# Performance work log

Hardware: AMD Instinct MI355X
Metric: run time of the kernel (lower is better)

## Reference

```python
import jax, jax.numpy as jnp
import numpy as np

PATCH = 16
TOP_K = 5
EPS = 1e-12


def l2_normalize(x, axis):
    sq = jnp.sum(x * x, axis=axis, keepdims=True)
    return x * jax.lax.rsqrt(jnp.maximum(sq, EPS))


def patch_embed(imgs, conv_w, conv_b):
    # imgs: (P, 3, 32, 32) -> (P, n_patches=4, D=768)
    y = jax.lax.conv_general_dilated(
        imgs, conv_w, window_strides=(PATCH, PATCH), padding='VALID',
        dimension_numbers=('NCHW', 'OIHW', 'NCHW'))  # (P, D, 2, 2)
    y = y + conv_b[None, :, None, None]
    P, D = y.shape[0], y.shape[1]
    return y.reshape(P, D, -1).transpose(0, 2, 1)  # (P, 4, D)


def setup_inputs() -> dict:
    key = jax.random.key(0)
    k1, k2, k3, k4 = jax.random.split(key, 4)
    B, N, D = 256, 196, 768
    P = 32  # pool_size
    x_embed = jax.random.normal(k1, (B, N, D), dtype=jnp.float32)
    # uniform(-1, 1) init as in the torch module
    prompt = jax.random.uniform(k2, (P, 3, 32, 32), dtype=jnp.float32, minval=-1.0, maxval=1.0)
    prompt_key = jax.random.uniform(k3, (P, D), dtype=jnp.float32, minval=-1.0, maxval=1.0)
    conv_w = jax.random.normal(k4, (D, 3, PATCH, PATCH), dtype=jnp.float32) * 0.02
    conv_b = jnp.zeros((D,), dtype=jnp.float32)
    return {'x_embed': x_embed, 'prompt': prompt, 'prompt_key': prompt_key,
            'conv_w': conv_w, 'conv_b': conv_b}


def reference(x_embed, prompt, prompt_key, conv_w, conv_b):
    B = x_embed.shape[0]
    prompt_embed = patch_embed(prompt, conv_w, conv_b)      # (P, 4, D)

    x_embed_mean = jnp.mean(x_embed, axis=1)                # (B, D), embedding_key='mean'
    prompt_norm = l2_normalize(prompt_key, axis=1)          # (P, D)
    x_embed_norm = l2_normalize(x_embed_mean, axis=1)       # (B, D)
    similarity = x_embed_norm @ prompt_norm.T               # (B, P)

    _, idx = jax.lax.top_k(similarity, TOP_K)               # (B, top_k)

    batched_prompt_embed = prompt_embed[idx]                # (B, top_k, 4, D)
    Bq, K, L, D = batched_prompt_embed.shape
    batched_prompt_embed = batched_prompt_embed.reshape(Bq, K * L, D)

    batched_key_norm = prompt_norm[idx]                     # (B, top_k, D)
    reduce_sim = jnp.sum(batched_key_norm * x_embed_norm[:, None, :]) / B

    prompted_embedding = jnp.concatenate([batched_prompt_embed, x_embed], axis=1)
    return prompted_embedding, reduce_sim, similarity, idx
```

## Files before the change

### kernel.cpp

```cpp
#include <hip/hip_runtime.h>

typedef float __attribute__((ext_vector_type(4))) f32x4;

#define BB 256
#define NN 196
#define DD 768
#define PP 32
#define TOPK 5
#define NROW 216

#define OUT0_ELTS (BB * NROW * DD)
#define RS_OFF    OUT0_ELTS
#define SIM_OFF   (OUT0_ELTS + 1)
#define IDX_OFF   (OUT0_ELTS + 1 + BB * PP)

#define WS_PEMB   0

__global__ __launch_bounds__(256) void k_prep(const float* __restrict__ prompt,
                                              const float* __restrict__ cw,
                                              const float* __restrict__ cb,
                                              float* __restrict__ pemb) {
    const int t = threadIdx.x;
    const int bxx = blockIdx.x;
    const int chunk = bxx / 32, pg = bxx - chunk * 32;
    const int m0 = pg * 4;
    const int n = chunk * 256 + t;
    __shared__ float patch[4 * DD];
    for (int idx = t; idx < 4 * DD; idx += 256) {
        const int j = idx / DD, kk = idx - j * DD;
        const int c = kk >> 8, rem = kk & 255;
        const int kh = rem >> 4, kw = rem & 15;
        const int m = m0 + j;
        const int p = m >> 2, l = m & 3;
        patch[idx] = prompt[(size_t)p * 3072 + (size_t)c * 1024
                            + ((l >> 1) * 16 + kh) * 32 + (l & 1) * 16 + kw];
    }
    __syncthreads();
    const float4* wrow = (const float4*)(cw + (size_t)n * DD);
    const float4* p0 = (const float4*)(patch);
    const float4* p1 = (const float4*)(patch + DD);
    const float4* p2 = (const float4*)(patch + 2 * DD);
    const float4* p3 = (const float4*)(patch + 3 * DD);
    float a0 = 0.f, a1 = 0.f, a2 = 0.f, a3 = 0.f;
#pragma unroll 4
    for (int kk = 0; kk < 192; ++kk) {
        const float4 w = wrow[kk];
        const float4 q0 = p0[kk], q1 = p1[kk], q2 = p2[kk], q3 = p3[kk];
        a0 += q0.x * w.x + q0.y * w.y + q0.z * w.z + q0.w * w.w;
        a1 += q1.x * w.x + q1.y * w.y + q1.z * w.z + q1.w * w.w;
        a2 += q2.x * w.x + q2.y * w.y + q2.z * w.z + q2.w * w.w;
        a3 += q3.x * w.x + q3.y * w.y + q3.z * w.z + q3.w * w.w;
    }
    const float bias = cb[n];
    pemb[(size_t)(m0 + 0) * DD + n] = a0 + bias;
    pemb[(size_t)(m0 + 1) * DD + n] = a1 + bias;
    pemb[(size_t)(m0 + 2) * DD + n] = a2 + bias;
    pemb[(size_t)(m0 + 3) * DD + n] = a3 + bias;
}

__global__ __launch_bounds__(768) void k_fused(const float* __restrict__ x,
                                               const float* __restrict__ pkey,
                                               const float* __restrict__ pemb,
                                               float* __restrict__ out) {
    const int b = blockIdx.x;
    const int t = threadIdx.x;
    const int g = t / 192, c = t - g * 192;
    const float* xb = x + (size_t)b * (NN * DD);
    float* ob = out + (size_t)b * (NROW * DD) + 20 * DD;
    f32x4 s = (f32x4)(0.f);
    f32x4 va[7], vb[7];
#pragma unroll
    for (int i = 0; i < 7; ++i)
        va[i] = __builtin_nontemporal_load((const f32x4*)(xb + (size_t)(g + 4 * i) * DD) + c);
#pragma unroll
    for (int o = 0; o < 7; ++o) {
        if (o < 6) {
#pragma unroll
            for (int i = 0; i < 7; ++i) {
                const int row = g + 4 * ((o + 1) * 7 + i);
                vb[i] = __builtin_nontemporal_load((const f32x4*)(xb + (size_t)row * DD) + c);
            }
        }
#pragma unroll
        for (int i = 0; i < 7; ++i) {
            const int row = g + 4 * (o * 7 + i);
            s += va[i];
            __builtin_nontemporal_store(va[i], (f32x4*)(ob + (size_t)row * DD) + c);
        }
#pragma unroll
        for (int i = 0; i < 7; ++i) va[i] = vb[i];
    }
    __shared__ f32x4 comb[768];
    __shared__ float xm[768];
    __shared__ float sims[PP];
    __shared__ float wred[12];
    __shared__ float rsh;
    __shared__ int lidx[TOPK];
    comb[g * 192 + c] = s;
    __syncthreads();
    if (g == 0) {
        f32x4 s0 = comb[c], s1 = comb[192 + c], s2 = comb[384 + c], s3 = comb[576 + c];
        f32x4 m4 = (s0 + s1 + s2 + s3) * (1.0f / NN);
        xm[4 * c + 0] = m4.x;
        xm[4 * c + 1] = m4.y;
        xm[4 * c + 2] = m4.z;
        xm[4 * c + 3] = m4.w;
    }
    __syncthreads();
    float sq = xm[t] * xm[t];
#pragma unroll
    for (int off = 32; off; off >>= 1) sq += __shfl_down(sq, off);
    if ((t & 63) == 0) wred[t >> 6] = sq;
    __syncthreads();
    if (t == 0) {
        float tot = 0.f;
        for (int i = 0; i < 12; ++i) tot += wred[i];
        rsh = rsqrtf(fmaxf(tot, 1e-12f));
    }
    __syncthreads();
    const float r = rsh;
    if (t < 512) {
        const int p = t >> 4, sub = t & 15;
        const float* pr = pkey + (size_t)p * DD;
        float acc = 0.f, nrm = 0.f;
#pragma unroll 8
        for (int j = 0; j < 48; ++j) {
            const int k = sub + (j << 4);
            const float pk = pr[k];
            acc += xm[k] * pk;
            nrm += pk * pk;
        }
        acc += __shfl_down(acc, 8, 16);  nrm += __shfl_down(nrm, 8, 16);
        acc += __shfl_down(acc, 4, 16);  nrm += __shfl_down(nrm, 4, 16);
        acc += __shfl_down(acc, 2, 16);  nrm += __shfl_down(nrm, 2, 16);
        acc += __shfl_down(acc, 1, 16);  nrm += __shfl_down(nrm, 1, 16);
        if (sub == 0) {
            const float sv = acc * rsqrtf(fmaxf(nrm, 1e-12f)) * r;
            sims[p] = sv;
            out[SIM_OFF + b * PP + p] = sv;
        }
    }
    __syncthreads();
    if (t < 64) {
        float v = (t < PP) ? sims[t] : -1e30f;
        float rsum = 0.f;
#pragma unroll
        for (int k = 0; k < TOPK; ++k) {
            float bv = v; int bbi = t;
#pragma unroll
            for (int off = 32; off; off >>= 1) {
                const float ov = __shfl_xor(bv, off);
                const int   oi = __shfl_xor(bbi, off);
                if (ov > bv || (ov == bv && oi < bbi)) { bv = ov; bbi = oi; }
            }
            if (t == 0) {
                lidx[k] = bbi;
                out[IDX_OFF + b * TOPK + k] = (float)bbi;
                rsum += bv;
            }
            if (t == bbi) v = -1e30f;
        }
        if (t == 0) atomicAdd(&out[RS_OFF], rsum * (1.0f / BB));
    }
    __syncthreads();
    f32x4* dst = (f32x4*)(out + (size_t)b * (NROW * DD));
    const f32x4* src = (const f32x4*)pemb;
    for (int v = t; v < 20 * 192; v += 768) {
        const int row = v / 192;
        const int off = v - row * 192;
        const int srow = lidx[row >> 2] * 4 + (row & 3);
        __builtin_nontemporal_store(src[srow * 192 + off], dst + row * 192 + off);
    }
}

extern "C" void kernel_launch(void* const* d_in, const int* in_sizes, int n_in,
                              void* d_out, int out_size, void* d_ws, size_t ws_size,
                              hipStream_t stream) {
    const float* x      = (const float*)d_in[0];
    const float* prompt = (const float*)d_in[1];
    const float* pkey   = (const float*)d_in[2];
    const float* cw     = (const float*)d_in[3];
    const float* cb     = (const float*)d_in[4];
    float* out = (float*)d_out;
    char* ws = (char*)d_ws;

    float* pemb = (float*)(ws + WS_PEMB);

    hipMemsetAsync(out + RS_OFF, 0, sizeof(float), stream);
    k_prep<<<96, 256, 0, stream>>>(prompt, cw, cb, pemb);
    k_fused<<<BB, 768, 0, stream>>>(x, pkey, pemb, out);
}
```

Baseline: 331.3 us.

## Split row copy across two blocks per batch and merge patch-embed into copy kernel

```diff
diff --git a/kernel.cpp b/kernel.cpp
--- a/kernel.cpp
+++ b/kernel.cpp
@@ -16,98 +16,97 @@
 
 #define WS_PEMB   0
 
-__global__ __launch_bounds__(256) void k_prep(const float* __restrict__ prompt,
-                                              const float* __restrict__ cw,
-                                              const float* __restrict__ cb,
-                                              float* __restrict__ pemb) {
+__global__ __launch_bounds__(768, 6) void k_copy(
+    const float* __restrict__ x, const float* __restrict__ prompt,
+    const float* __restrict__ cw, const float* __restrict__ cb,
+    float* __restrict__ pemb, float* __restrict__ out)
+{
     const int t = threadIdx.x;
-    const int bxx = blockIdx.x;
-    const int chunk = bxx / 32, pg = bxx - chunk * 32;
-    const int m0 = pg * 4;
-    const int n = chunk * 256 + t;
-    __shared__ float patch[4 * DD];
-    for (int idx = t; idx < 4 * DD; idx += 256) {
-        const int j = idx / DD, kk = idx - j * DD;
-        const int c = kk >> 8, rem = kk & 255;
-        const int kh = rem >> 4, kw = rem & 15;
-        const int m = m0 + j;
-        const int p = m >> 2, l = m & 3;
-        patch[idx] = prompt[(size_t)p * 3072 + (size_t)c * 1024
-                            + ((l >> 1) * 16 + kh) * 32 + (l & 1) * 16 + kw];
+    __shared__ f32x4 shbuf4[768];
+
+    if (blockIdx.x < PP) {
+        const int p = blockIdx.x;
+        float* patch = (float*)shbuf4;
+        for (int idx = t; idx < 4 * DD; idx += 768) {
+            const int j = idx / DD, kk = idx - j * DD;
+            const int ch = kk >> 8, rem = kk & 255;
+            const int kh = rem >> 4, kw = rem & 15;
+            patch[idx] = prompt[(size_t)p * 3072 + (size_t)ch * 1024
+                                + ((j >> 1) * 16 + kh) * 32 + (j & 1) * 16 + kw];
+        }
+        __syncthreads();
+        const float4* wrow = (const float4*)(cw + (size_t)t * DD);
+        const float4* q0 = (const float4*)(patch);
+        const float4* q1 = (const float4*)(patch + DD);
+        const float4* q2 = (const float4*)(patch + 2 * DD);
+        const float4* q3 = (const float4*)(patch + 3 * DD);
+        float a0 = 0.f, a1 = 0.f, a2 = 0.f, a3 = 0.f;
+#pragma unroll 4
+        for (int kk = 0; kk < 192; ++kk) {
+            const float4 w = wrow[kk];
+            const float4 v0 = q0[kk], v1 = q1[kk], v2 = q2[kk], v3 = q3[kk];
+            a0 += v0.x * w.x + v0.y * w.y + v0.z * w.z + v0.w * w.w;
+            a1 += v1.x * w.x + v1.y * w.y + v1.z * w.z + v1.w * w.w;
+            a2 += v2.x * w.x + v2.y * w.y + v2.z * w.z + v2.w * w.w;
+            a3 += v3.x * w.x + v3.y * w.y + v3.z * w.z + v3.w * w.w;
+        }
+        const float bias = cb[t];
+        float* pe = pemb + (size_t)(4 * p) * DD + t;
+        pe[0]      = a0 + bias;
+        pe[DD]     = a1 + bias;
+        pe[2 * DD] = a2 + bias;
+        pe[3 * DD] = a3 + bias;
+        return;
     }
+
+    const int blk = blockIdx.x - PP;
+    const int b = blk >> 1, h = blk & 1;
+    const int g = t / 192, c = t - g * 192;
+    const int r0 = h * 98;
+    const f32x4* xb4 = (const f32x4*)(x + (size_t)b * (NN * DD));
+    f32x4* ob4 = (f32x4*)(out + (size_t)b * (NROW * DD) + 20 * DD);
+    f32x4 s = (f32x4)(0.f);
+#pragma unroll
+    for (int o = 0; o < 5; ++o) {
+        f32x4 vv[5];
+#pragma unroll
+        for (int i = 0; i < 5; ++i) {
+            const int r = g + 4 * (o * 5 + i);
+            if (r < 98)
+                vv[i] = __builtin_nontemporal_load(xb4 + (size_t)(r0 + r) * 192 + c);
+        }
+#pragma unroll
+        for (int i = 0; i < 5; ++i) {
+            const int r = g + 4 * (o * 5 + i);
+            if (r < 98) {
+                s += vv[i];
+                __builtin_nontemporal_store(vv[i], ob4 + (size_t)(r0 + r) * 192 + c);
+            }
+        }
+    }
+    shbuf4[g * 192 + c] = s;
     __syncthreads();
-    const float4* wrow = (const float4*)(cw + (size_t)n * DD);
-    const float4* p0 = (const float4*)(patch);
-    const float4* p1 = (const float4*)(patch + DD);
-    const float4* p2 = (const float4*)(patch + 2 * DD);
-    const float4* p3 = (const float4*)(patch + 3 * DD);
-    float a0 = 0.f, a1 = 0.f, a2 = 0.f, a3 = 0.f;
-#pragma unroll 4
-    for (int kk = 0; kk < 192; ++kk) {
-        const float4 w = wrow[kk];
-        const float4 q0 = p0[kk], q1 = p1[kk], q2 = p2[kk], q3 = p3[kk];
-        a0 += q0.x * w.x + q0.y * w.y + q0.z * w.z + q0.w * w.w;
-        a1 += q1.x * w.x + q1.y * w.y + q1.z * w.z + q1.w * w.w;
-        a2 += q2.x * w.x + q2.y * w.y + q2.z * w.z + q2.w * w.w;
-        a3 += q3.x * w.x + q3.y * w.y + q3.z * w.z + q3.w * w.w;
+    if (t < 192) {
+        const f32x4 ps = shbuf4[t] + shbuf4[192 + t] + shbuf4[384 + t] + shbuf4[576 + t];
+        ((f32x4*)(out + (size_t)b * (NROW * DD) + (size_t)h * DD))[t] = ps;
     }
-    const float bias = cb[n];
-    pemb[(size_t)(m0 + 0) * DD + n] = a0 + bias;
-    pemb[(size_t)(m0 + 1) * DD + n] = a1 + bias;
-    pemb[(size_t)(m0 + 2) * DD + n] = a2 + bias;
-    pemb[(size_t)(m0 + 3) * DD + n] = a3 + bias;
 }
 
-__global__ __launch_bounds__(768) void k_fused(const float* __restrict__ x,
-                                               const float* __restrict__ pkey,
-                                               const float* __restrict__ pemb,
-                                               float* __restrict__ out) {
+__global__ __launch_bounds__(768) void k_tail(const float* __restrict__ pkey,
+                                              const float* __restrict__ pemb,
+                                              float* __restrict__ out) {
     const int b = blockIdx.x;
     const int t = threadIdx.x;
-    const int g = t / 192, c = t - g * 192;
-    const float* xb = x + (size_t)b * (NN * DD);
-    float* ob = out + (size_t)b * (NROW * DD) + 20 * DD;
-    f32x4 s = (f32x4)(0.f);
-    f32x4 va[7], vb[7];
-#pragma unroll
-    for (int i = 0; i < 7; ++i)
-        va[i] = __builtin_nontemporal_load((const f32x4*)(xb + (size_t)(g + 4 * i) * DD) + c);
-#pragma unroll
-    for (int o = 0; o < 7; ++o) {
-        if (o < 6) {
-#pragma unroll
-            for (int i = 0; i < 7; ++i) {
-                const int row = g + 4 * ((o + 1) * 7 + i);
-                vb[i] = __builtin_nontemporal_load((const f32x4*)(xb + (size_t)row * DD) + c);
-            }
-        }
-#pragma unroll
-        for (int i = 0; i < 7; ++i) {
-            const int row = g + 4 * (o * 7 + i);
-            s += va[i];
-            __builtin_nontemporal_store(va[i], (f32x4*)(ob + (size_t)row * DD) + c);
-        }
-#pragma unroll
-        for (int i = 0; i < 7; ++i) va[i] = vb[i];
-    }
-    __shared__ f32x4 comb[768];
     __shared__ float xm[768];
     __shared__ float sims[PP];
     __shared__ float wred[12];
     __shared__ float rsh;
     __shared__ int lidx[TOPK];
-    comb[g * 192 + c] = s;
-    __syncthreads();
-    if (g == 0) {
-        f32x4 s0 = comb[c], s1 = comb[192 + c], s2 = comb[384 + c], s3 = comb[576 + c];
-        f32x4 m4 = (s0 + s1 + s2 + s3) * (1.0f / NN);
-        xm[4 * c + 0] = m4.x;
-        xm[4 * c + 1] = m4.y;
-        xm[4 * c + 2] = m4.z;
-        xm[4 * c + 3] = m4.w;
-    }
-    __syncthreads();
-    float sq = xm[t] * xm[t];
+
+    const float* sc = out + (size_t)b * (NROW * DD);
+    const float xmv = (sc[t] + sc[DD + t]) * (1.0f / NN);
+    xm[t] = xmv;
+    float sq = xmv * xmv;
 #pragma unroll
     for (int off = 32; off; off >>= 1) sq += __shfl_down(sq, off);
     if ((t & 63) == 0) wred[t >> 6] = sq;
@@ -119,6 +118,7 @@
     }
     __syncthreads();
     const float r = rsh;
+
     if (t < 512) {
         const int p = t >> 4, sub = t & 15;
         const float* pr = pkey + (size_t)p * DD;
@@ -141,6 +141,7 @@
         }
     }
     __syncthreads();
+
     if (t < 64) {
         float v = (t < PP) ? sims[t] : -1e30f;
         float rsum = 0.f;
@@ -163,6 +164,7 @@
         if (t == 0) atomicAdd(&out[RS_OFF], rsum * (1.0f / BB));
     }
     __syncthreads();
+
     f32x4* dst = (f32x4*)(out + (size_t)b * (NROW * DD));
     const f32x4* src = (const f32x4*)pemb;
     for (int v = t; v < 20 * 192; v += 768) {
@@ -187,6 +189,6 @@
     float* pemb = (float*)(ws + WS_PEMB);
 
     hipMemsetAsync(out + RS_OFF, 0, sizeof(float), stream);
-    k_prep<<<96, 256, 0, stream>>>(prompt, cw, cb, pemb);
-    k_fused<<<BB, 768, 0, stream>>>(x, pkey, pemb, out);
+    k_copy<<<PP + 2 * BB, 768, 0, stream>>>(x, prompt, cw, cb, pemb, out);
+    k_tail<<<BB, 768, 0, stream>>>(pkey, pemb, out);
 }
```

Measured after the change: 358.8 us. 8.3% more time.
